# Kernel optimization log

Measured on AMD Instinct MI355X. Metric: run time of the kernel, lower is better.

## Reference

```python
import jax, jax.numpy as jnp
import numpy as np

N, E = 50000, 800000
F_IN, F_EDGE = 64, 16
HEADS, C_HEAD = 4, 32
HC = HEADS * C_HEAD  # 128 = hidden_node_channels
MLP_IN = F_IN + HC   # 192
MLP0, MLP1 = 128, 128
NEG_SLOPE = 0.2


def leaky_relu(x):
    return jnp.where(x >= 0, x, NEG_SLOPE * x)


def layer_norm(x, g, b, eps=1e-5):
    mu = jnp.mean(x, axis=-1, keepdims=True)
    var = jnp.mean(jnp.square(x - mu), axis=-1, keepdims=True)
    return (x - mu) * jax.lax.rsqrt(var + eps) * g + b


def setup_inputs() -> dict:
    key = jax.random.key(0)
    ks = jax.random.split(key, 24)
    s = 0.05
    inp = {
        "node_features": jax.random.normal(ks[0], (N, F_IN), jnp.float32),
        "edge_features": jax.random.normal(ks[1], (E, F_EDGE), jnp.float32),
        "edge_index": jax.random.randint(ks[2], (2, E), 0, N, jnp.int32),
        # GATv2Conv params (share_weights=False, bias=True, edge_dim=16)
        "W_l": jax.random.normal(ks[3], (F_IN, HC), jnp.float32) * s,
        "b_l": jax.random.normal(ks[4], (HC,), jnp.float32) * s,
        "W_r": jax.random.normal(ks[5], (F_IN, HC), jnp.float32) * s,
        "b_r": jax.random.normal(ks[6], (HC,), jnp.float32) * s,
        "W_e": jax.random.normal(ks[7], (F_EDGE, HC), jnp.float32) * s,
        "att": jax.random.normal(ks[8], (HEADS, C_HEAD), jnp.float32) * s,
        "gat_bias": jax.random.normal(ks[9], (HC,), jnp.float32) * s,
        # residual_connection: Linear(64->128) + LayerNorm
        "res_W": jax.random.normal(ks[10], (F_IN, MLP1), jnp.float32) * s,
        "res_b": jax.random.normal(ks[11], (MLP1,), jnp.float32) * s,
        "res_g": 1.0 + jax.random.normal(ks[12], (MLP1,), jnp.float32) * s,
        "res_beta": jax.random.normal(ks[13], (MLP1,), jnp.float32) * s,
        # upd MLP: two ffn_blocks (Linear -> LayerNorm -> ReLU)
        "W0": jax.random.normal(ks[14], (MLP_IN, MLP0), jnp.float32) * s,
        "b0": jax.random.normal(ks[15], (MLP0,), jnp.float32) * s,
        "g0": 1.0 + jax.random.normal(ks[16], (MLP0,), jnp.float32) * s,
        "beta0": jax.random.normal(ks[17], (MLP0,), jnp.float32) * s,
        "W1": jax.random.normal(ks[18], (MLP0, MLP1), jnp.float32) * s,
        "b1": jax.random.normal(ks[19], (MLP1,), jnp.float32) * s,
        "g1": 1.0 + jax.random.normal(ks[20], (MLP1,), jnp.float32) * s,
        "beta1": jax.random.normal(ks[21], (MLP1,), jnp.float32) * s,
    }
    return inp


def reference(node_features, edge_features, edge_index,
              W_l, b_l, W_r, b_r, W_e, att, gat_bias,
              res_W, res_b, res_g, res_beta,
              W0, b0, g0, beta0, W1, b1, g1, beta1):
    src, dst = edge_index[0], edge_index[1]

    # ---- GATv2Conv ----
    x_l = (node_features @ W_l + b_l).reshape(N, HEADS, C_HEAD)  # source transform
    x_r = (node_features @ W_r + b_r).reshape(N, HEADS, C_HEAD)  # target transform
    e = (edge_features @ W_e).reshape(E, HEADS, C_HEAD)

    x_j = x_l[src]                      # [E,H,C] messages
    m = x_j + x_r[dst] + e              # [E,H,C]
    logits = jnp.sum(leaky_relu(m) * att, axis=-1)  # [E,H]

    # segment softmax over incoming edges of each destination node
    mx = jax.ops.segment_max(logits, dst, num_segments=N)      # [N,H]
    ex = jnp.exp(logits - mx[dst])                             # [E,H]
    den = jax.ops.segment_sum(ex, dst, num_segments=N)         # [N,H]
    alpha = ex / den[dst]                                      # [E,H]

    agg = jax.ops.segment_sum(alpha[..., None] * x_j, dst, num_segments=N)
    gat_out = agg.reshape(N, HC) + gat_bias                    # [N,128]

    # ---- residual concat-MLP ----
    identity = layer_norm(node_features @ res_W + res_b, res_g, res_beta)
    h = jnp.concatenate([node_features, gat_out], axis=-1)     # [N,192]
    h = jax.nn.relu(layer_norm(h @ W0 + b0, g0, beta0))
    h = jax.nn.relu(layer_norm(h @ W1 + b1, g1, beta1))
    return identity + h
```

## Files before the change

### kernel.cpp

```cpp
#include <hip/hip_runtime.h>

#define NN 50000
#define NE 800000
#define NB 196
#define K1B 782

typedef __attribute__((ext_vector_type(8))) short bf16x8;
typedef __attribute__((ext_vector_type(4))) float f32x4;
typedef __attribute__((ext_vector_type(2))) _Float16 h2f;

__device__ __forceinline__ int rfl(int v) { return __builtin_amdgcn_readfirstlane(v); }

__device__ __forceinline__ unsigned short bfb(float x) {
    union { float f; unsigned u; } v; v.f = x;
    unsigned r = v.u + 0x7FFFu + ((v.u >> 16) & 1u);
    return (unsigned short)(r >> 16);
}
__device__ __forceinline__ unsigned pkbf(float lo, float hi) {
    return ((unsigned)bfb(hi) << 16) | (unsigned)bfb(lo);
}
__device__ __forceinline__ unsigned pkh2(float a, float b) {
    union { h2f h; unsigned u; } x;
    x.h.x = (_Float16)a; x.h.y = (_Float16)b;
    return x.u;
}
__device__ __forceinline__ float fdot2u(unsigned a, unsigned b, float c) {
    union { unsigned u; h2f h; } ua, ub; ua.u = a; ub.u = b;
    return __builtin_amdgcn_fdot2(ua.h, ub.h, c, false);
}

__device__ __forceinline__ float dpp_reduce16(float p) {
    int t;
    t = __builtin_amdgcn_update_dpp(0, __float_as_int(p), 0xB1, 0xF, 0xF, false);
    p += __int_as_float(t);
    t = __builtin_amdgcn_update_dpp(0, __float_as_int(p), 0x4E, 0xF, 0xF, false);
    p += __int_as_float(t);
    t = __builtin_amdgcn_update_dpp(0, __float_as_int(p), 0x124, 0xF, 0xF, false);
    p += __int_as_float(t);
    t = __builtin_amdgcn_update_dpp(0, __float_as_int(p), 0x128, 0xF, 0xF, false);
    p += __int_as_float(t);
    return p;
}

__device__ __forceinline__ float exp2_hw(float x) {
    float r;
    asm("v_exp_f32 %0, %1" : "=v"(r) : "v"(x));
    return r;
}

__global__ __launch_bounds__(256) void k0_prep(
    const float* __restrict__ W_l, const float* __restrict__ W_r,
    const float* __restrict__ res_W, const float* __restrict__ W0,
    const float* __restrict__ W1, const float* __restrict__ W_e,
    unsigned short* __restrict__ Wtl, unsigned short* __restrict__ Wtr,
    unsigned short* __restrict__ Wtres, unsigned short* __restrict__ Wt0,
    unsigned short* __restrict__ Wt1,
    unsigned* __restrict__ Wep,
    int* __restrict__ deg, int* __restrict__ row_start)
{
    const int t0 = blockIdx.x * 256 + threadIdx.x;
    if (t0 < 24576) { int n = t0 / 192, k = t0 - n * 192; Wt0[t0] = bfb(W0[k * 128 + n]); }
    if (t0 < 16384) { int n = t0 >> 7, k = t0 & 127; Wt1[t0] = bfb(W1[k * 128 + n]); }
    if (t0 < 8192) {
        int n = t0 >> 6, k = t0 & 63;
        Wtl[t0]   = bfb(W_l[k * 128 + n]);
        Wtr[t0]   = bfb(W_r[k * 128 + n]);
        Wtres[t0] = bfb(res_W[k * 128 + n]);
    }
    if (t0 < 1024) {
        int c = t0 >> 3, j = t0 & 7;
        Wep[t0] = pkh2(W_e[(2 * j) * 128 + c], W_e[(2 * j + 1) * 128 + c]);
    }
    if (t0 < NN) deg[t0] = 0;
    if (t0 == 0) row_start[NN] = NE;
}

__global__ __launch_bounds__(256, 4) void ka_nodes_degree(
    const float* __restrict__ nf,
    const unsigned short* __restrict__ Wtl, const float* __restrict__ b_l,
    const unsigned short* __restrict__ Wtr, const float* __restrict__ b_r,
    const unsigned short* __restrict__ Wtres, const float* __restrict__ res_b,
    const float* __restrict__ res_g, const float* __restrict__ res_beta,
    unsigned* __restrict__ xlp, float* __restrict__ x_r, float* __restrict__ ident,
    const int* __restrict__ eidx, int* __restrict__ deg, int* __restrict__ rank,
    const float* __restrict__ ef, unsigned* __restrict__ efp)
{
    if (blockIdx.x >= K1B) {
        int e = (blockIdx.x - K1B) * 256 + threadIdx.x;
        if (e < NE) {
            rank[e] = atomicAdd(deg + eidx[NE + e], 1);
            const float4* er = (const float4*)(ef + (size_t)e * 16);
            float4 v0 = er[0], v1 = er[1], v2 = er[2], v3 = er[3];
            uint4 o0, o1;
            o0.x = pkh2(v0.x, v0.y); o0.y = pkh2(v0.z, v0.w);
            o0.z = pkh2(v1.x, v1.y); o0.w = pkh2(v1.z, v1.w);
            o1.x = pkh2(v2.x, v2.y); o1.y = pkh2(v2.z, v2.w);
            o1.z = pkh2(v3.x, v3.y); o1.w = pkh2(v3.z, v3.w);
            *(uint4*)(efp + (size_t)e * 8)     = o0;
            *(uint4*)(efp + (size_t)e * 8 + 4) = o1;
        }
        return;
    }
    __shared__ __align__(16) unsigned As32[64 * 36];
    const int tid = threadIdx.x;
    const int node0 = blockIdx.x * 64;

    for (int i = tid; i < 64 * 32; i += 256) {
        int n = i >> 5, c2 = i & 31;
        int gn = node0 + n;
        float2 v = make_float2(0.f, 0.f);
        if (gn < NN) v = *(const float2*)(nf + gn * 64 + 2 * c2);
        As32[n * 36 + c2] = pkbf(v.x, v.y);
    }
    __syncthreads();

    const int lane = tid & 63, w = tid >> 6;
    const int c = lane & 15, ko = lane >> 4;
    const unsigned short* As = (const unsigned short*)As32;
    bf16x8 a0 = *(const bf16x8*)(As + (w * 16 + c) * 72 + 0 * 32 + ko * 8);
    bf16x8 a1 = *(const bf16x8*)(As + (w * 16 + c) * 72 + 1 * 32 + ko * 8);
    const int lrow0 = node0 + w * 16 + 4 * ko;

    #pragma unroll
    for (int p = 0; p < 3; ++p) {
        const unsigned short* Wt = (p == 0) ? Wtl : (p == 1) ? Wtr : Wtres;
        f32x4 acc[8];
        #pragma unroll
        for (int nt = 0; nt < 8; ++nt) acc[nt] = f32x4{0.f, 0.f, 0.f, 0.f};
        #pragma unroll
        for (int nt = 0; nt < 8; ++nt) {
            bf16x8 bf0 = *(const bf16x8*)(Wt + (nt * 16 + c) * 64 + 0 * 32 + ko * 8);
            acc[nt] = __builtin_amdgcn_mfma_f32_16x16x32_bf16(a0, bf0, acc[nt], 0, 0, 0);
            bf16x8 bf1 = *(const bf16x8*)(Wt + (nt * 16 + c) * 64 + 1 * 32 + ko * 8);
            acc[nt] = __builtin_amdgcn_mfma_f32_16x16x32_bf16(a1, bf1, acc[nt], 0, 0, 0);
        }
        if (p == 0) {
            float bv[8];
            #pragma unroll
            for (int nt = 0; nt < 8; ++nt) bv[nt] = b_l[nt * 16 + c];
            #pragma unroll
            for (int reg = 0; reg < 4; ++reg) {
                int row = lrow0 + reg;
                #pragma unroll
                for (int nt = 0; nt < 8; ++nt) {
                    float v = acc[nt][reg] + bv[nt];
                    float v2 = __shfl_xor(v, 1, 64);
                    if (row < NN && (lane & 1) == 0)
                        xlp[row * 64 + nt * 8 + (c >> 1)] = pkh2(v, v2);
                }
            }
        } else if (p == 1) {
            float bv[8];
            #pragma unroll
            for (int nt = 0; nt < 8; ++nt) bv[nt] = b_r[nt * 16 + c];
            #pragma unroll
            for (int reg = 0; reg < 4; ++reg) {
                int row = lrow0 + reg;
                if (row < NN) {
                    #pragma unroll
                    for (int nt = 0; nt < 8; ++nt)
                        x_r[row * 128 + nt * 16 + c] = acc[nt][reg] + bv[nt];
                }
            }
        } else {
            float bv[8], gv[8], tv[8];
            #pragma unroll
            for (int nt = 0; nt < 8; ++nt) {
                bv[nt] = res_b[nt * 16 + c];
                gv[nt] = res_g[nt * 16 + c];
                tv[nt] = res_beta[nt * 16 + c];
            }
            #pragma unroll
            for (int reg = 0; reg < 4; ++reg) {
                float sum = 0.f, sq = 0.f, hv[8];
                #pragma unroll
                for (int nt = 0; nt < 8; ++nt) {
                    float v = acc[nt][reg] + bv[nt];
                    hv[nt] = v; sum += v; sq += v * v;
                }
                #pragma unroll
                for (int m = 1; m <= 8; m <<= 1) {
                    sum += __shfl_xor(sum, m, 64);
                    sq  += __shfl_xor(sq, m, 64);
                }
                float mean = sum * (1.f / 128.f);
                float inv  = rsqrtf(sq * (1.f / 128.f) - mean * mean + 1e-5f);
                int row = lrow0 + reg;
                if (row < NN) {
                    #pragma unroll
                    for (int nt = 0; nt < 8; ++nt)
                        ident[row * 128 + nt * 16 + c] =
                            (hv[nt] - mean) * inv * gv[nt] + tv[nt];
                }
            }
        }
    }
}

__global__ __launch_bounds__(256) void k3a_blocksum(
    const int* __restrict__ deg, int* __restrict__ bsum)
{
    __shared__ int ws[4];
    int i = blockIdx.x * 256 + threadIdx.x;
    int v = (i < NN) ? deg[i] : 0;
    #pragma unroll
    for (int m = 32; m >= 1; m >>= 1) v += __shfl_xor(v, m, 64);
    if ((threadIdx.x & 63) == 0) ws[threadIdx.x >> 6] = v;
    __syncthreads();
    if (threadIdx.x == 0) bsum[blockIdx.x] = ws[0] + ws[1] + ws[2] + ws[3];
}

__global__ __launch_bounds__(256) void k3c_apply(
    const int* __restrict__ deg, const int* __restrict__ bsum,
    int* __restrict__ row_start)
{
    __shared__ int wsum[4];
    __shared__ int roff[4];
    const int tid = threadIdx.x, lane = tid & 63, wid = tid >> 6;
    int bv = (tid < blockIdx.x) ? bsum[tid] : 0;
    #pragma unroll
    for (int m = 32; m >= 1; m >>= 1) bv += __shfl_xor(bv, m, 64);
    if (lane == 0) roff[wid] = bv;

    int i = blockIdx.x * 256 + tid;
    int v = (i < NN) ? deg[i] : 0;
    int sc = v;
    #pragma unroll
    for (int m = 1; m < 64; m <<= 1) {
        int t = __shfl_up(sc, m, 64);
        if (lane >= m) sc += t;
    }
    if (lane == 63) wsum[wid] = sc;
    __syncthreads();
    int off = roff[0] + roff[1] + roff[2] + roff[3];
    for (int w = 0; w < wid; ++w) off += wsum[w];
    int excl = off + sc - v;
    if (i < NN) row_start[i] = excl;
}

__global__ __launch_bounds__(256) void k4_scatter(
    const int* __restrict__ eidx, const int* __restrict__ row_start,
    const int* __restrict__ rank, int2* __restrict__ csr_es)
{
    int e = blockIdx.x * 256 + threadIdx.x;
    if (e >= NE) return;
    int dst = eidx[NE + e];
    csr_es[row_start[dst] + rank[e]] = make_int2(e, eidx[e]);
}

__global__ __launch_bounds__(256, 4) void k5_attn_aggregate(
    const int2* __restrict__ csr_es, const int* __restrict__ row_start,
    const unsigned* __restrict__ efp, const unsigned* __restrict__ Wep,
    const float* __restrict__ att,
    const unsigned* __restrict__ xlp, const float* __restrict__ x_r,
    const float* __restrict__ gat_bias,
    float* __restrict__ gat_out)
{
    const int lane = threadIdx.x & 63;
    const int node = (blockIdx.x * 256 + threadIdx.x) >> 6;
    if (node >= NN) return;
    const int c = lane * 2;

    uint4 t0 = *(const uint4*)(Wep + c * 8);
    uint4 t1 = *(const uint4*)(Wep + c * 8 + 4);
    uint4 t2 = *(const uint4*)(Wep + (c + 1) * 8);
    uint4 t3 = *(const uint4*)(Wep + (c + 1) * 8 + 4);
    unsigned wx0 = t0.x, wx1 = t0.y, wx2 = t0.z, wx3 = t0.w;
    unsigned wx4 = t1.x, wx5 = t1.y, wx6 = t1.z, wx7 = t1.w;
    unsigned wy0 = t2.x, wy1 = t2.y, wy2 = t2.z, wy3 = t2.w;
    unsigned wy4 = t3.x, wy5 = t3.y, wy6 = t3.z, wy7 = t3.w;

    const float LOG2E = 1.44269504088896340736f;
    float2 a2 = *(const float2*)(att + c);
    a2.x *= LOG2E; a2.y *= LOG2E;
    const float2 xr = *(const float2*)(x_r + node * 128 + c);
    const uint4* __restrict__ efq = (const uint4*)efp;
    const unsigned* __restrict__ xlc = xlp + lane;

    const int sj  = rfl(row_start[node]);
    const int epj = rfl(row_start[node + 1]);

    float den = 0.f, n0 = 0.f, n1 = 0.f;

    for (int base = sj; base < epj; base += 64) {
        const int cnt = min(64, epj - base);
        int pidx = base + lane; if (pidx > NE - 1) pidx = NE - 1;
        const int2 mc = csr_es[pidx];

        uint4 aE0, aE1, bE0, bE1, cE0, cE1, dE0, dE1, eE0, eE1, fE0, fE1;
        unsigned aX, bX, cX, dX, eX, fX;

#define LOADS(E0_, E1_, X_, K_)                                            \
        { int kk = (K_); if (kk >= cnt) kk = cnt - 1;                      \
          int eid  = __builtin_amdgcn_readlane(mc.x, kk);                  \
          int srcn = __builtin_amdgcn_readlane(mc.y, kk);                  \
          E0_ = efq[eid * 2 + 0]; E1_ = efq[eid * 2 + 1];                  \
          X_  = xlc[srcn * 64]; }

#define CONSUME(E0_, E1_, X_)                                              \
        { asm volatile("" : "+v"(wx0), "+v"(wx1), "+v"(wx2), "+v"(wx3),    \
                            "+v"(wx4), "+v"(wx5), "+v"(wx6), "+v"(wx7));   \
          asm volatile("" : "+v"(wy0), "+v"(wy1), "+v"(wy2), "+v"(wy3),    \
                            "+v"(wy4), "+v"(wy5), "+v"(wy6), "+v"(wy7));   \
          union { unsigned u; h2f h; } ux; ux.u = (X_);                    \
          float cx0 = (float)ux.h.x, cx1 = (float)ux.h.y;                  \
          float ax = cx0 + xr.x;                                           \
          float ay = cx1 + xr.y;                                           \
          float bx = 0.f, by = 0.f;                                        \
          ax = fdot2u((E0_).x, wx0, ax);  ay = fdot2u((E0_).x, wy0, ay);   \
          bx = fdot2u((E0_).y, wx1, bx);  by = fdot2u((E0_).y, wy1, by);   \
          ax = fdot2u((E0_).z, wx2, ax);  ay = fdot2u((E0_).z, wy2, ay);   \
          bx = fdot2u((E0_).w, wx3, bx);  by = fdot2u((E0_).w, wy3, by);   \
          ax = fdot2u((E1_).x, wx4, ax);  ay = fdot2u((E1_).x, wy4, ay);   \
          bx = fdot2u((E1_).y, wx5, bx);  by = fdot2u((E1_).y, wy5, by);   \
          ax = fdot2u((E1_).z, wx6, ax);  ay = fdot2u((E1_).z, wy6, ay);   \
          bx = fdot2u((E1_).w, wx7, bx);  by = fdot2u((E1_).w, wy7, by);   \
          float evx = ax + bx;                                             \
          float evy = ay + by;                                             \
          float lx = fmaxf(evx, 0.2f * evx);                               \
          float ly = fmaxf(evy, 0.2f * evy);                               \
          float p = lx * a2.x + ly * a2.y;                                 \
          p = dpp_reduce16(p);                                             \
          float ev = exp2_hw(p);                                           \
          den += ev; n0 += ev * cx0; n1 += ev * cx1; }

        LOADS(aE0, aE1, aX, 0);
        LOADS(bE0, bE1, bX, 1);
        LOADS(cE0, cE1, cX, 2);
        LOADS(dE0, dE1, dX, 3);
        LOADS(eE0, eE1, eX, 4);
        int j = 0;
        while (j + 6 <= cnt) {
            LOADS(fE0, fE1, fX, j + 5);
            CONSUME(aE0, aE1, aX);
            LOADS(aE0, aE1, aX, j + 6);
            CONSUME(bE0, bE1, bX);
            LOADS(bE0, bE1, bX, j + 7);
            CONSUME(cE0, cE1, cX);
            LOADS(cE0, cE1, cX, j + 8);
            CONSUME(dE0, dE1, dX);
            LOADS(dE0, dE1, dX, j + 9);
            CONSUME(eE0, eE1, eX);
            LOADS(eE0, eE1, eX, j + 10);
            CONSUME(fE0, fE1, fX);
            j += 6;
        }
        if (j < cnt)     CONSUME(aE0, aE1, aX);
        if (j + 1 < cnt) CONSUME(bE0, bE1, bX);
        if (j + 2 < cnt) CONSUME(cE0, cE1, cX);
        if (j + 3 < cnt) CONSUME(dE0, dE1, dX);
        if (j + 4 < cnt) CONSUME(eE0, eE1, eX);
#undef LOADS
#undef CONSUME
    }
    float rden = (den > 0.f) ? (1.f / den) : 0.f;
    float2 gb = *(const float2*)(gat_bias + c);
    float2 o; o.x = n0 * rden + gb.x; o.y = n1 * rden + gb.y;
    *(float2*)(gat_out + node * 128 + c) = o;
}

__global__ __launch_bounds__(256, 4) void k6_mlp_mfma(
    const float* __restrict__ nf, const float* __restrict__ gat,
    const float* __restrict__ ident,
    const unsigned short* __restrict__ Wt0, const float* __restrict__ b0,
    const float* __restrict__ g0, const float* __restrict__ be0,
    const unsigned short* __restrict__ Wt1, const float* __restrict__ b1,
    const float* __restrict__ g1, const float* __restrict__ be1,
    float* __restrict__ out)
{
    __shared__ __align__(16) unsigned LDS[64 * 100];
    const int tid = threadIdx.x;
    const int node0 = blockIdx.x * 64;

    for (int i = tid; i < 64 * 96; i += 256) {
        int n = i / 96, c2 = i - n * 96;
        int gn = node0 + n;
        float2 v = make_float2(0.f, 0.f);
        if (gn < NN)
            v = (c2 < 32) ? *(const float2*)(nf + gn * 64 + 2 * c2)
                          : *(const float2*)(gat + gn * 128 + 2 * (c2 - 32));
        LDS[n * 100 + c2] = pkbf(v.x, v.y);
    }
    __syncthreads();

    const int lane = tid & 63, w = tid >> 6;
    const int c = lane & 15, ko = lane >> 4;
    const int lrow = w * 16 + 4 * ko;

    f32x4 acc[8];
    #pragma unroll
    for (int nt = 0; nt < 8; ++nt) acc[nt] = f32x4{0.f, 0.f, 0.f, 0.f};

    #pragma unroll
    for (int kb = 0; kb < 6; ++kb) {
        bf16x8 a = *(const bf16x8*)((const unsigned short*)LDS +
                                    (w * 16 + c) * 200 + kb * 32 + ko * 8);
        #pragma unroll
        for (int nt = 0; nt < 8; ++nt) {
            bf16x8 b = *(const bf16x8*)(Wt0 + (nt * 16 + c) * 192 + kb * 32 + ko * 8);
            acc[nt] = __builtin_amdgcn_mfma_f32_16x16x32_bf16(a, b, acc[nt], 0, 0, 0);
        }
    }

    float bv[8], gv[8], tv[8];
    #pragma unroll
    for (int nt = 0; nt < 8; ++nt) {
        bv[nt] = b0[nt * 16 + c];
        gv[nt] = g0[nt * 16 + c];
        tv[nt] = be0[nt * 16 + c];
    }
    __syncthreads();

    unsigned short* Hs = (unsigned short*)LDS;
    #pragma unroll
    for (int reg = 0; reg < 4; ++reg) {
        float sum = 0.f, sq = 0.f, hv[8];
        #pragma unroll
        for (int nt = 0; nt < 8; ++nt) {
            float v = acc[nt][reg] + bv[nt];
            hv[nt] = v; sum += v; sq += v * v;
        }
        #pragma unroll
        for (int m = 1; m <= 8; m <<= 1) {
            sum += __shfl_xor(sum, m, 64);
            sq  += __shfl_xor(sq, m, 64);
        }
        float mean = sum * (1.f / 128.f);
        float inv  = rsqrtf(sq * (1.f / 128.f) - mean * mean + 1e-5f);
        #pragma unroll
        for (int nt = 0; nt < 8; ++nt) {
            float h = fmaxf((hv[nt] - mean) * inv * gv[nt] + tv[nt], 0.f);
            Hs[(lrow + reg) * 136 + nt * 16 + c] = bfb(h);
        }
    }
    __syncthreads();

    #pragma unroll
    for (int nt = 0; nt < 8; ++nt) acc[nt] = f32x4{0.f, 0.f, 0.f, 0.f};
    #pragma unroll
    for (int kb = 0; kb < 4; ++kb) {
        bf16x8 a = *(const bf16x8*)((const unsigned short*)LDS +
                                    (w * 16 + c) * 136 + kb * 32 + ko * 8);
        #pragma unroll
        for (int nt = 0; nt < 8; ++nt) {
            bf16x8 b = *(const bf16x8*)(Wt1 + (nt * 16 + c) * 128 + kb * 32 + ko * 8);
            acc[nt] = __builtin_amdgcn_mfma_f32_16x16x32_bf16(a, b, acc[nt], 0, 0, 0);
        }
    }

    #pragma unroll
    for (int nt = 0; nt < 8; ++nt) {
        bv[nt] = b1[nt * 16 + c];
        gv[nt] = g1[nt * 16 + c];
        tv[nt] = be1[nt * 16 + c];
    }
    #pragma unroll
    for (int reg = 0; reg < 4; ++reg) {
        float sum = 0.f, sq = 0.f, hv[8];
        #pragma unroll
        for (int nt = 0; nt < 8; ++nt) {
            float v = acc[nt][reg] + bv[nt];
            hv[nt] = v; sum += v; sq += v * v;
        }
        #pragma unroll
        for (int m = 1; m <= 8; m <<= 1) {
            sum += __shfl_xor(sum, m, 64);
            sq  += __shfl_xor(sq, m, 64);
        }
        float mean = sum * (1.f / 128.f);
        float inv  = rsqrtf(sq * (1.f / 128.f) - mean * mean + 1e-5f);
        int row = node0 + lrow + reg;
        if (row < NN) {
            #pragma unroll
            for (int nt = 0; nt < 8; ++nt) {
                float h = fmaxf((hv[nt] - mean) * inv * gv[nt] + tv[nt], 0.f);
                int col = nt * 16 + c;
                out[row * 128 + col] = ident[row * 128 + col] + h;
            }
        }
    }
}

extern "C" void kernel_launch(void* const* d_in, const int* in_sizes, int n_in,
                              void* d_out, int out_size, void* d_ws, size_t ws_size,
                              hipStream_t stream)
{
    const float* nf       = (const float*)d_in[0];
    const float* ef       = (const float*)d_in[1];
    const int*   eidx     = (const int*)d_in[2];
    const float* W_l      = (const float*)d_in[3];
    const float* b_l      = (const float*)d_in[4];
    const float* W_r      = (const float*)d_in[5];
    const float* b_r      = (const float*)d_in[6];
    const float* W_e      = (const float*)d_in[7];
    const float* att      = (const float*)d_in[8];
    const float* gat_bias = (const float*)d_in[9];
    const float* res_W    = (const float*)d_in[10];
    const float* res_b    = (const float*)d_in[11];
    const float* res_g    = (const float*)d_in[12];
    const float* res_beta = (const float*)d_in[13];
    const float* W0       = (const float*)d_in[14];
    const float* b0       = (const float*)d_in[15];
    const float* g0       = (const float*)d_in[16];
    const float* beta0    = (const float*)d_in[17];
    const float* W1       = (const float*)d_in[18];
    const float* b1       = (const float*)d_in[19];
    const float* g1       = (const float*)d_in[20];
    const float* beta1    = (const float*)d_in[21];
    float* out = (float*)d_out;

    char* ws = (char*)d_ws;
    size_t off = 0;
    auto alloc = [&](size_t bytes) -> void* {
        void* p = ws + off;
        off += (bytes + 255) & ~(size_t)255;
        return p;
    };
    unsigned* xlp  = (unsigned*)alloc((size_t)NN * 64 * 4);
    float* x_r     = (float*)alloc((size_t)NN * 128 * 4);
    float* ident   = (float*)alloc((size_t)NN * 128 * 4);
    int* deg       = (int*)alloc((size_t)NN * 4);
    int* row_start = (int*)alloc((size_t)(NN + 1) * 4);
    int* rank      = (int*)alloc((size_t)NE * 4);
    int* bsum      = (int*)alloc((size_t)(NB + 1) * 4);
    int2* csr_es   = (int2*)alloc((size_t)NE * 8);
    float* gat_out = (float*)alloc((size_t)NN * 128 * 4);
    unsigned short* Wtl   = (unsigned short*)alloc(8192 * 2);
    unsigned short* Wtr   = (unsigned short*)alloc(8192 * 2);
    unsigned short* Wtres = (unsigned short*)alloc(8192 * 2);
    unsigned short* Wt0   = (unsigned short*)alloc(24576 * 2);
    unsigned short* Wt1   = (unsigned short*)alloc(16384 * 2);
    unsigned* Wep = (unsigned*)alloc(1024 * 4);
    unsigned* efp = (unsigned*)alloc((size_t)NE * 8 * 4);

    k0_prep<<<NB, 256, 0, stream>>>(W_l, W_r, res_W, W0, W1, W_e,
                                    Wtl, Wtr, Wtres, Wt0, Wt1, Wep,
                                    deg, row_start);

    ka_nodes_degree<<<K1B + (NE + 255) / 256, 256, 0, stream>>>(
        nf, Wtl, b_l, Wtr, b_r, Wtres, res_b, res_g, res_beta,
        xlp, x_r, ident, eidx, deg, rank, ef, efp);

    k3a_blocksum<<<NB, 256, 0, stream>>>(deg, bsum);
    k3c_apply<<<NB, 256, 0, stream>>>(deg, bsum, row_start);

    k4_scatter<<<(NE + 255) / 256, 256, 0, stream>>>(eidx, row_start, rank, csr_es);

    k5_attn_aggregate<<<(NN * 64 + 255) / 256, 256, 0, stream>>>(
        csr_es, row_start, efp, Wep, att, xlp, x_r, gat_bias, gat_out);

    k6_mlp_mfma<<<(NN + 63) / 64, 256, 0, stream>>>(
        nf, gat_out, ident, Wt0, b0, g0, beta0, Wt1, b1, g1, beta1, out);
}
```

Baseline: 331.4 us.

## Move residual projection into MLP kernel and store intermediates in half precision

The residual Linear+LayerNorm is moved from the node-transform kernel into the final MLP kernel, where it reuses the node features already staged in LDS. This removes the fp32 identity buffer round trip. x_r is now stored as packed fp16 and gat_out as packed bf16, roughly halving intermediate traffic. The trade-off is more register pressure in the MLP kernel (launch bounds drop from 4 to 3 waves) and extra rounding of x_r and gat_out.

```diff
diff --git a/kernel.cpp b/kernel.cpp
--- a/kernel.cpp
+++ b/kernel.cpp
@@ -79,9 +79,7 @@
     const float* __restrict__ nf,
     const unsigned short* __restrict__ Wtl, const float* __restrict__ b_l,
     const unsigned short* __restrict__ Wtr, const float* __restrict__ b_r,
-    const unsigned short* __restrict__ Wtres, const float* __restrict__ res_b,
-    const float* __restrict__ res_g, const float* __restrict__ res_beta,
-    unsigned* __restrict__ xlp, float* __restrict__ x_r, float* __restrict__ ident,
+    unsigned* __restrict__ xlp, unsigned* __restrict__ xrp,
     const int* __restrict__ eidx, int* __restrict__ deg, int* __restrict__ rank,
     const float* __restrict__ ef, unsigned* __restrict__ efp)
 {
@@ -122,8 +120,10 @@
     const int lrow0 = node0 + w * 16 + 4 * ko;
 
     #pragma unroll
-    for (int p = 0; p < 3; ++p) {
-        const unsigned short* Wt = (p == 0) ? Wtl : (p == 1) ? Wtr : Wtres;
+    for (int p = 0; p < 2; ++p) {
+        const unsigned short* Wt = (p == 0) ? Wtl : Wtr;
+        const float* bias = (p == 0) ? b_l : b_r;
+        unsigned* outp = (p == 0) ? xlp : xrp;
         f32x4 acc[8];
         #pragma unroll
         for (int nt = 0; nt < 8; ++nt) acc[nt] = f32x4{0.f, 0.f, 0.f, 0.f};
@@ -134,64 +134,18 @@
             bf16x8 bf1 = *(const bf16x8*)(Wt + (nt * 16 + c) * 64 + 1 * 32 + ko * 8);
             acc[nt] = __builtin_amdgcn_mfma_f32_16x16x32_bf16(a1, bf1, acc[nt], 0, 0, 0);
         }
-        if (p == 0) {
-            float bv[8];
-            #pragma unroll
-            for (int nt = 0; nt < 8; ++nt) bv[nt] = b_l[nt * 16 + c];
-            #pragma unroll
-            for (int reg = 0; reg < 4; ++reg) {
-                int row = lrow0 + reg;
-                #pragma unroll
-                for (int nt = 0; nt < 8; ++nt) {
-                    float v = acc[nt][reg] + bv[nt];
-                    float v2 = __shfl_xor(v, 1, 64);
-                    if (row < NN && (lane & 1) == 0)
-                        xlp[row * 64 + nt * 8 + (c >> 1)] = pkh2(v, v2);
-                }
-            }
-        } else if (p == 1) {
-            float bv[8];
-            #pragma unroll
-            for (int nt = 0; nt < 8; ++nt) bv[nt] = b_r[nt * 16 + c];
-            #pragma unroll
-            for (int reg = 0; reg < 4; ++reg) {
-                int row = lrow0 + reg;
-                if (row < NN) {
-                    #pragma unroll
-                    for (int nt = 0; nt < 8; ++nt)
-                        x_r[row * 128 + nt * 16 + c] = acc[nt][reg] + bv[nt];
-                }
-            }
-        } else {
-            float bv[8], gv[8], tv[8];
+        float bv[8];
+        #pragma unroll
+        for (int nt = 0; nt < 8; ++nt) bv[nt] = bias[nt * 16 + c];
+        #pragma unroll
+        for (int reg = 0; reg < 4; ++reg) {
+            int row = lrow0 + reg;
             #pragma unroll
             for (int nt = 0; nt < 8; ++nt) {
-                bv[nt] = res_b[nt * 16 + c];
-                gv[nt] = res_g[nt * 16 + c];
-                tv[nt] = res_beta[nt * 16 + c];
-            }
-            #pragma unroll
-            for (int reg = 0; reg < 4; ++reg) {
-                float sum = 0.f, sq = 0.f, hv[8];
-                #pragma unroll
-                for (int nt = 0; nt < 8; ++nt) {
-                    float v = acc[nt][reg] + bv[nt];
-                    hv[nt] = v; sum += v; sq += v * v;
-                }
-                #pragma unroll
-                for (int m = 1; m <= 8; m <<= 1) {
-                    sum += __shfl_xor(sum, m, 64);
-                    sq  += __shfl_xor(sq, m, 64);
-                }
-                float mean = sum * (1.f / 128.f);
-                float inv  = rsqrtf(sq * (1.f / 128.f) - mean * mean + 1e-5f);
-                int row = lrow0 + reg;
-                if (row < NN) {
-                    #pragma unroll
-                    for (int nt = 0; nt < 8; ++nt)
-                        ident[row * 128 + nt * 16 + c] =
-                            (hv[nt] - mean) * inv * gv[nt] + tv[nt];
-                }
+                float v = acc[nt][reg] + bv[nt];
+                float v2 = __shfl_xor(v, 1, 64);
+                if (row < NN && (lane & 1) == 0)
+                    outp[row * 64 + nt * 8 + (c >> 1)] = pkh2(v, v2);
             }
         }
     }
@@ -252,9 +206,9 @@
     const int2* __restrict__ csr_es, const int* __restrict__ row_start,
     const unsigned* __restrict__ efp, const unsigned* __restrict__ Wep,
     const float* __restrict__ att,
-    const unsigned* __restrict__ xlp, const float* __restrict__ x_r,
+    const unsigned* __restrict__ xlp, const unsigned* __restrict__ xrp,
     const float* __restrict__ gat_bias,
-    float* __restrict__ gat_out)
+    unsigned* __restrict__ gatp)
 {
     const int lane = threadIdx.x & 63;
     const int node = (blockIdx.x * 256 + threadIdx.x) >> 6;
@@ -273,7 +227,12 @@
     const float LOG2E = 1.44269504088896340736f;
     float2 a2 = *(const float2*)(att + c);
     a2.x *= LOG2E; a2.y *= LOG2E;
-    const float2 xr = *(const float2*)(x_r + node * 128 + c);
+    float2 xr;
+    {
+        union { unsigned u; h2f h; } uxr;
+        uxr.u = xrp[node * 64 + lane];
+        xr.x = (float)uxr.h.x; xr.y = (float)uxr.h.y;
+    }
     const uint4* __restrict__ efq = (const uint4*)efp;
     const unsigned* __restrict__ xlc = xlp + lane;
 
@@ -355,13 +314,14 @@
     }
     float rden = (den > 0.f) ? (1.f / den) : 0.f;
     float2 gb = *(const float2*)(gat_bias + c);
-    float2 o; o.x = n0 * rden + gb.x; o.y = n1 * rden + gb.y;
-    *(float2*)(gat_out + node * 128 + c) = o;
-}
-
-__global__ __launch_bounds__(256, 4) void k6_mlp_mfma(
-    const float* __restrict__ nf, const float* __restrict__ gat,
-    const float* __restrict__ ident,
+    float ox = n0 * rden + gb.x, oy = n1 * rden + gb.y;
+    gatp[node * 64 + lane] = pkbf(ox, oy);
+}
+
+__global__ __launch_bounds__(256, 3) void k6_mlp_mfma(
+    const float* __restrict__ nf, const unsigned* __restrict__ gatp,
+    const unsigned short* __restrict__ Wtres, const float* __restrict__ res_b,
+    const float* __restrict__ res_g, const float* __restrict__ res_be,
     const unsigned short* __restrict__ Wt0, const float* __restrict__ b0,
     const float* __restrict__ g0, const float* __restrict__ be0,
     const unsigned short* __restrict__ Wt1, const float* __restrict__ b1,
@@ -375,11 +335,16 @@
     for (int i = tid; i < 64 * 96; i += 256) {
         int n = i / 96, c2 = i - n * 96;
         int gn = node0 + n;
-        float2 v = make_float2(0.f, 0.f);
-        if (gn < NN)
-            v = (c2 < 32) ? *(const float2*)(nf + gn * 64 + 2 * c2)
-                          : *(const float2*)(gat + gn * 128 + 2 * (c2 - 32));
-        LDS[n * 100 + c2] = pkbf(v.x, v.y);
+        unsigned pv = 0u;
+        if (gn < NN) {
+            if (c2 < 32) {
+                float2 v = *(const float2*)(nf + gn * 64 + 2 * c2);
+                pv = pkbf(v.x, v.y);
+            } else {
+                pv = gatp[gn * 64 + (c2 - 32)];
+            }
+        }
+        LDS[n * 100 + c2] = pv;
     }
     __syncthreads();
 
@@ -387,10 +352,23 @@
     const int c = lane & 15, ko = lane >> 4;
     const int lrow = w * 16 + 4 * ko;
 
+    f32x4 accr[8];
+    #pragma unroll
+    for (int nt = 0; nt < 8; ++nt) accr[nt] = f32x4{0.f, 0.f, 0.f, 0.f};
+    #pragma unroll
+    for (int kb = 0; kb < 2; ++kb) {
+        bf16x8 a = *(const bf16x8*)((const unsigned short*)LDS +
+                                    (w * 16 + c) * 200 + kb * 32 + ko * 8);
+        #pragma unroll
+        for (int nt = 0; nt < 8; ++nt) {
+            bf16x8 b = *(const bf16x8*)(Wtres + (nt * 16 + c) * 64 + kb * 32 + ko * 8);
+            accr[nt] = __builtin_amdgcn_mfma_f32_16x16x32_bf16(a, b, accr[nt], 0, 0, 0);
+        }
+    }
+
     f32x4 acc[8];
     #pragma unroll
     for (int nt = 0; nt < 8; ++nt) acc[nt] = f32x4{0.f, 0.f, 0.f, 0.f};
-
     #pragma unroll
     for (int kb = 0; kb < 6; ++kb) {
         bf16x8 a = *(const bf16x8*)((const unsigned short*)LDS +
@@ -448,34 +426,46 @@
         }
     }
 
+    float bvr[8], gvr[8], tvr[8];
     #pragma unroll
     for (int nt = 0; nt < 8; ++nt) {
-        bv[nt] = b1[nt * 16 + c];
-        gv[nt] = g1[nt * 16 + c];
-        tv[nt] = be1[nt * 16 + c];
+        bv[nt]  = b1[nt * 16 + c];
+        gv[nt]  = g1[nt * 16 + c];
+        tv[nt]  = be1[nt * 16 + c];
+        bvr[nt] = res_b[nt * 16 + c];
+        gvr[nt] = res_g[nt * 16 + c];
+        tvr[nt] = res_be[nt * 16 + c];
     }
     #pragma unroll
     for (int reg = 0; reg < 4; ++reg) {
         float sum = 0.f, sq = 0.f, hv[8];
+        float sumr = 0.f, sqr = 0.f, rv[8];
         #pragma unroll
         for (int nt = 0; nt < 8; ++nt) {
             float v = acc[nt][reg] + bv[nt];
             hv[nt] = v; sum += v; sq += v * v;
+            float u = accr[nt][reg] + bvr[nt];
+            rv[nt] = u; sumr += u; sqr += u * u;
         }
         #pragma unroll
         for (int m = 1; m <= 8; m <<= 1) {
-            sum += __shfl_xor(sum, m, 64);
-            sq  += __shfl_xor(sq, m, 64);
-        }
-        float mean = sum * (1.f / 128.f);
-        float inv  = rsqrtf(sq * (1.f / 128.f) - mean * mean + 1e-5f);
+            sum  += __shfl_xor(sum, m, 64);
+            sq   += __shfl_xor(sq, m, 64);
+            sumr += __shfl_xor(sumr, m, 64);
+            sqr  += __shfl_xor(sqr, m, 64);
+        }
+        float mean  = sum  * (1.f / 128.f);
+        float inv   = rsqrtf(sq  * (1.f / 128.f) - mean  * mean  + 1e-5f);
+        float meanr = sumr * (1.f / 128.f);
+        float invr  = rsqrtf(sqr * (1.f / 128.f) - meanr * meanr + 1e-5f);
         int row = node0 + lrow + reg;
         if (row < NN) {
             #pragma unroll
             for (int nt = 0; nt < 8; ++nt) {
-                float h = fmaxf((hv[nt] - mean) * inv * gv[nt] + tv[nt], 0.f);
+                float h  = fmaxf((hv[nt] - mean) * inv * gv[nt] + tv[nt], 0.f);
+                float id = (rv[nt] - meanr) * invr * gvr[nt] + tvr[nt];
                 int col = nt * 16 + c;
-                out[row * 128 + col] = ident[row * 128 + col] + h;
+                out[row * 128 + col] = id + h;
             }
         }
     }
@@ -517,14 +507,13 @@
         return p;
     };
     unsigned* xlp  = (unsigned*)alloc((size_t)NN * 64 * 4);
-    float* x_r     = (float*)alloc((size_t)NN * 128 * 4);
-    float* ident   = (float*)alloc((size_t)NN * 128 * 4);
+    unsigned* xrp  = (unsigned*)alloc((size_t)NN * 64 * 4);
     int* deg       = (int*)alloc((size_t)NN * 4);
     int* row_start = (int*)alloc((size_t)(NN + 1) * 4);
     int* rank      = (int*)alloc((size_t)NE * 4);
     int* bsum      = (int*)alloc((size_t)(NB + 1) * 4);
     int2* csr_es   = (int2*)alloc((size_t)NE * 8);
-    float* gat_out = (float*)alloc((size_t)NN * 128 * 4);
+    unsigned* gatp = (unsigned*)alloc((size_t)NN * 64 * 4);
     unsigned short* Wtl   = (unsigned short*)alloc(8192 * 2);
     unsigned short* Wtr   = (unsigned short*)alloc(8192 * 2);
     unsigned short* Wtres = (unsigned short*)alloc(8192 * 2);
@@ -538,8 +527,8 @@
                                     deg, row_start);
 
     ka_nodes_degree<<<K1B + (NE + 255) / 256, 256, 0, stream>>>(
-        nf, Wtl, b_l, Wtr, b_r, Wtres, res_b, res_g, res_beta,
-        xlp, x_r, ident, eidx, deg, rank, ef, efp);
+        nf, Wtl, b_l, Wtr, b_r,
+        xlp, xrp, eidx, deg, rank, ef, efp);
 
     k3a_blocksum<<<NB, 256, 0, stream>>>(deg, bsum);
     k3c_apply<<<NB, 256, 0, stream>>>(deg, bsum, row_start);
@@ -547,8 +536,9 @@
     k4_scatter<<<(NE + 255) / 256, 256, 0, stream>>>(eidx, row_start, rank, csr_es);
 
     k5_attn_aggregate<<<(NN * 64 + 255) / 256, 256, 0, stream>>>(
-        csr_es, row_start, efp, Wep, att, xlp, x_r, gat_bias, gat_out);
+        csr_es, row_start, efp, Wep, att, xlp, xrp, gat_bias, gatp);
 
     k6_mlp_mfma<<<(NN + 63) / 64, 256, 0, stream>>>(
-        nf, gat_out, ident, Wt0, b0, g0, beta0, Wt1, b1, g1, beta1, out);
-}
+        nf, gatp, Wtres, res_b, res_g, res_beta,
+        Wt0, b0, g0, beta0, Wt1, b1, g1, beta1, out);
+}
```

New measurement: 340.0 us. 2.6% more time.
